# Kernel optimization log

Measured on AMD Instinct MI355X. Metric: run time of the kernel, lower is better.

## Reference

```python
import jax, jax.numpy as jnp
import numpy as np
from jax import lax

NUM_STEPS = 20
BATCH, DIM, HID = 4096, 512, 2048


def setup_inputs() -> dict:
    key = jax.random.key(0)
    k_z, k_w1, k_w2 = jax.random.split(key, 3)
    z0 = jax.random.normal(k_z, (BATCH, DIM), dtype=jnp.float32)
    # fan-in scaled weights so the ODE dynamics stay well-conditioned
    W1 = jax.random.normal(k_w1, (DIM + 1, HID), dtype=jnp.float32) * (1.0 / np.sqrt(DIM + 1))
    b1 = jnp.zeros((HID,), dtype=jnp.float32)
    W2 = jax.random.normal(k_w2, (HID, DIM), dtype=jnp.float32) * (0.1 / np.sqrt(HID))
    b2 = jnp.zeros((DIM,), dtype=jnp.float32)
    t0 = jnp.zeros((), dtype=jnp.float32)
    t1 = jnp.ones((), dtype=jnp.float32)
    return {"z0": z0, "W1": W1, "b1": b1, "W2": W2, "b2": b2, "t0": t0, "t1": t1}


def reference(z0, W1, b1, W2, b2, t0, t1):
    h = (t1 - t0) / NUM_STEPS

    def func(z, t):
        # time broadcast to [batch, 1], concatenated to the state (Neural-ODE MLP dynamics)
        tb = jnp.full((z.shape[0], 1), t, dtype=z.dtype)
        hidden = jnp.tanh(jnp.concatenate([z, tb], axis=-1) @ W1 + b1)
        return hidden @ W2 + b2

    def step(z, i):
        t = t0 + i * h
        k1 = func(z, t)
        k2 = func(z + 0.5 * h * k1, t + 0.5 * h)
        k3 = func(z + 0.5 * h * k2, t + 0.5 * h)
        k4 = func(z + h * k3, t + h)
        z_next = z + (h / 6.0) * (k1 + 2.0 * k2 + 2.0 * k3 + k4)
        return z_next, None

    z, _ = lax.scan(step, z0, jnp.arange(NUM_STEPS, dtype=z0.dtype))
    return z
```

## Files before the change

### kernel.cpp

```cpp
#include <hip/hip_runtime.h>
#include <hip/hip_bf16.h>

#define BATCH 4096
#define DIM   512
#define HID   2048
#define NSTEPS 20

typedef __attribute__((ext_vector_type(8))) short short8;
typedef __attribute__((ext_vector_type(4))) short short4v;
typedef __attribute__((ext_vector_type(4))) float floatx4;

#define GLL(dst, src) __builtin_amdgcn_global_load_lds( \
    (const __attribute__((address_space(1))) void*)(src), \
    (__attribute__((address_space(3))) void*)(dst), 16, 0, 0)

__device__ __forceinline__ short f2bf(float x) {
    union { float f; unsigned u; } v; v.f = x;
    unsigned r = v.u + 0x7fffu + ((v.u >> 16) & 1u);
    return (short)(r >> 16);
}

__device__ __forceinline__ float fast_tanh(float x) {
    float e = __builtin_amdgcn_exp2f(x * 2.8853900817779268f);
    float r = __builtin_amdgcn_rcpf(1.0f + e);
    return 1.0f - 2.0f * r;
}

__global__ void transpose_cvt(const float* __restrict__ src, short* __restrict__ dst,
                              int K, int N) {
    __shared__ float tile[32][33];
    int k0 = blockIdx.x * 32, n0 = blockIdx.y * 32;
    int tx = threadIdx.x, ty = threadIdx.y;
    #pragma unroll
    for (int r = ty; r < 32; r += 8)
        tile[r][tx] = src[(size_t)(k0 + r) * N + n0 + tx];
    __syncthreads();
    #pragma unroll
    for (int r = ty; r < 32; r += 8)
        dst[(size_t)(n0 + r) * K + k0 + tx] = f2bf(tile[tx][r]);
}

__global__ void extract_row(const float* __restrict__ W1, float* __restrict__ w1last) {
    int i = blockIdx.x * 256 + threadIdx.x;
    w1last[i] = W1[(size_t)DIM * HID + i];
}

__global__ void init_abuf(const float* __restrict__ z0, short* __restrict__ abuf) {
    size_t i = (size_t)(blockIdx.x * 256 + threadIdx.x) * 4;
    float4 zv = *(const float4*)(z0 + i);
    short4v o;
    o[0] = f2bf(zv.x); o[1] = f2bf(zv.y); o[2] = f2bf(zv.z); o[3] = f2bf(zv.w);
    *(short4v*)(abuf + i) = o;
}

__global__ __launch_bounds__(256, 2)
void gemm1_tanh(const short* __restrict__ A, const short* __restrict__ Bt,
                const float* __restrict__ b1, const float* __restrict__ w1last,
                const float* __restrict__ t0p, const float* __restrict__ t1p,
                float c_t, float step_i,
                short* __restrict__ hidden) {
    __shared__ short Alds[128 * 128];
    __shared__ short Blds[128 * 128];
    const int tid = threadIdx.x;
    const int lane = tid & 63;
    const int wave = tid >> 6;
    const int wm = wave >> 1, wn = wave & 1;
    const int bm0 = blockIdx.x * 128;
    const int bn0 = blockIdx.y * 128;

    const float t0 = t0p[0], t1 = t1p[0];
    const float h = (t1 - t0) / (float)NSTEPS;
    const float teval = t0 + (step_i + c_t) * h;

    floatx4 acc[4][4];
    #pragma unroll
    for (int i = 0; i < 4; i++)
        #pragma unroll
        for (int j = 0; j < 4; j++) acc[i][j] = (floatx4)0.f;

    const int fr = lane & 15;
    const int fkc = lane >> 4;
    const int rx = fr & 7;

    for (int kk = 0; kk < DIM; kk += 128) {
        #pragma unroll
        for (int p = 0; p < 8; p++) {
            int c = tid + p * 256;
            int row = c >> 4;
            int ci = c & 15;
            int g = ((ci & 7) ^ (row & 7)) | (ci & 8);
            GLL(&Alds[c * 8], A  + (size_t)(bm0 + row) * DIM + kk + g * 8);
            GLL(&Blds[c * 8], Bt + (size_t)(bn0 + row) * DIM + kk + g * 8);
        }
        __syncthreads();
        #pragma unroll
        for (int s = 0; s < 4; s++) {
            const int lc = s * 4 + fkc;
            const int slot = ((((lc & 7) ^ rx) | (lc & 8))) * 8;
            short8 af[4], bfr[4];
            #pragma unroll
            for (int mt = 0; mt < 4; mt++)
                af[mt] = *(const short8*)&Alds[(wm * 64 + mt * 16 + fr) * 128 + slot];
            #pragma unroll
            for (int nt = 0; nt < 4; nt++)
                bfr[nt] = *(const short8*)&Blds[(wn * 64 + nt * 16 + fr) * 128 + slot];
            #pragma unroll
            for (int mt = 0; mt < 4; mt++)
                #pragma unroll
                for (int nt = 0; nt < 4; nt++)
                    acc[mt][nt] = __builtin_amdgcn_mfma_f32_16x16x32_bf16(bfr[nt], af[mt], acc[mt][nt], 0, 0, 0);
        }
        __syncthreads();
    }
    #pragma unroll
    for (int mt = 0; mt < 4; mt++) {
        int m = bm0 + wm * 64 + mt * 16 + fr;
        short* hrow = hidden + (size_t)m * HID;
        #pragma unroll
        for (int nt = 0; nt < 4; nt++) {
            int n0 = bn0 + wn * 64 + nt * 16 + fkc * 4;
            float4 bb = *(const float4*)&b1[n0];
            float4 wl = *(const float4*)&w1last[n0];
            short4v o;
            o[0] = f2bf(fast_tanh(acc[mt][nt][0] + bb.x + teval * wl.x));
            o[1] = f2bf(fast_tanh(acc[mt][nt][1] + bb.y + teval * wl.y));
            o[2] = f2bf(fast_tanh(acc[mt][nt][2] + bb.z + teval * wl.z));
            o[3] = f2bf(fast_tanh(acc[mt][nt][3] + bb.w + teval * wl.w));
            *(short4v*)&hrow[n0] = o;
        }
    }
}

__global__ __launch_bounds__(512, 2)
void gemm2_fused(const short* __restrict__ hidden,
                 const short* __restrict__ Bt,
                 const float* __restrict__ b2,
                 float* __restrict__ z,
                 float* __restrict__ kacc, short* __restrict__ abuf,
                 const float* __restrict__ t0p, const float* __restrict__ t1p,
                 int mode, float wk, float alpha_c) {
    __shared__ short lds[8 * 8192];
    const int tid = threadIdx.x;
    const int lane = tid & 63;
    const int wave = tid >> 6;
    const int bm0 = blockIdx.x * 64;
    const int bn0 = blockIdx.y * 64;
    const int kbase = wave * 256;

    short* slabA = &lds[wave * 8192];
    short* slabB = slabA + 4096;

    const int fr = lane & 15;
    const int fkc = lane >> 4;
    const int rx = fr & 7;
    const int l3 = lane >> 3;
    const int gch = (lane & 7) ^ l3;

    floatx4 acc[4][4];
    #pragma unroll
    for (int i = 0; i < 4; i++)
        #pragma unroll
        for (int j = 0; j < 4; j++) acc[i][j] = (floatx4)0.f;

    #pragma unroll
    for (int it = 0; it < 4; ++it) {
        const int k0 = kbase + it * 64;
        __builtin_amdgcn_s_waitcnt(0xC07F);
        #pragma unroll
        for (int j = 0; j < 8; j++) {
            int row = j * 8 + l3;
            GLL(&slabA[j * 512 + lane * 8], hidden + (size_t)(bm0 + row) * HID + k0 + gch * 8);
            GLL(&slabB[j * 512 + lane * 8], Bt     + (size_t)(bn0 + row) * HID + k0 + gch * 8);
        }
        __builtin_amdgcn_sched_barrier(0);
        __builtin_amdgcn_s_waitcnt(0x0F70);
        __builtin_amdgcn_sched_barrier(0);
        #pragma unroll
        for (int s = 0; s < 2; s++) {
            const int slot = ((s * 4 + fkc) ^ rx) * 8;
            short8 af[4], bfr[4];
            #pragma unroll
            for (int mt = 0; mt < 4; mt++)
                af[mt] = *(const short8*)&slabA[(mt * 16 + fr) * 64 + slot];
            #pragma unroll
            for (int nt = 0; nt < 4; nt++)
                bfr[nt] = *(const short8*)&slabB[(nt * 16 + fr) * 64 + slot];
            #pragma unroll
            for (int mt = 0; mt < 4; mt++)
                #pragma unroll
                for (int nt = 0; nt < 4; nt++)
                    acc[mt][nt] = __builtin_amdgcn_mfma_f32_16x16x32_bf16(af[mt], bfr[nt], acc[mt][nt], 0, 0, 0);
        }
        __builtin_amdgcn_sched_barrier(0);
    }

    float* fslab = (float*)slabA;
    #pragma unroll
    for (int mt = 0; mt < 4; mt++)
        #pragma unroll
        for (int nt = 0; nt < 4; nt++)
            #pragma unroll
            for (int r = 0; r < 4; r++) {
                int row = mt * 16 + fkc * 4 + r;
                int col = nt * 16 + fr;
                fslab[row * 64 + col] = acc[mt][nt][r];
            }
    __syncthreads();

    const int rrow = tid >> 3;
    const int c8 = (tid & 7) * 8;
    float4 v0 = make_float4(0.f, 0.f, 0.f, 0.f);
    float4 v1 = make_float4(0.f, 0.f, 0.f, 0.f);
    #pragma unroll
    for (int w = 0; w < 8; w++) {
        const float* fs = (const float*)&lds[w * 8192];
        float4 p0 = *(const float4*)&fs[rrow * 64 + c8];
        float4 p1 = *(const float4*)&fs[rrow * 64 + c8 + 4];
        v0.x += p0.x; v0.y += p0.y; v0.z += p0.z; v0.w += p0.w;
        v1.x += p1.x; v1.y += p1.y; v1.z += p1.z; v1.w += p1.w;
    }

    const float h = (t1p[0] - t0p[0]) / (float)NSTEPS;
    const float ah = alpha_c * h;
    const float h6 = h / 6.0f;
    const size_t base = (size_t)(bm0 + rrow) * DIM + bn0 + c8;
    float4 bb0 = *(const float4*)&b2[bn0 + c8];
    float4 bb1 = *(const float4*)&b2[bn0 + c8 + 4];
    float kv[8] = { v0.x + bb0.x, v0.y + bb0.y, v0.z + bb0.z, v0.w + bb0.w,
                    v1.x + bb1.x, v1.y + bb1.y, v1.z + bb1.z, v1.w + bb1.w };
    float4 zv0 = *(const float4*)&z[base];
    float4 zv1 = *(const float4*)&z[base + 4];
    float zl[8] = { zv0.x, zv0.y, zv0.z, zv0.w, zv1.x, zv1.y, zv1.z, zv1.w };
    float zn[8];
    if (mode == 0) {
        *(float4*)&kacc[base]     = make_float4(kv[0], kv[1], kv[2], kv[3]);
        *(float4*)&kacc[base + 4] = make_float4(kv[4], kv[5], kv[6], kv[7]);
        #pragma unroll
        for (int i = 0; i < 8; i++) zn[i] = zl[i] + ah * kv[i];
    } else if (mode == 1) {
        float4 ka0 = *(const float4*)&kacc[base];
        float4 ka1 = *(const float4*)&kacc[base + 4];
        *(float4*)&kacc[base]     = make_float4(ka0.x + wk * kv[0], ka0.y + wk * kv[1],
                                                ka0.z + wk * kv[2], ka0.w + wk * kv[3]);
        *(float4*)&kacc[base + 4] = make_float4(ka1.x + wk * kv[4], ka1.y + wk * kv[5],
                                                ka1.z + wk * kv[6], ka1.w + wk * kv[7]);
        #pragma unroll
        for (int i = 0; i < 8; i++) zn[i] = zl[i] + ah * kv[i];
    } else {
        float4 ka0 = *(const float4*)&kacc[base];
        float4 ka1 = *(const float4*)&kacc[base + 4];
        float kaf[8] = { ka0.x, ka0.y, ka0.z, ka0.w, ka1.x, ka1.y, ka1.z, ka1.w };
        #pragma unroll
        for (int i = 0; i < 8; i++) zn[i] = zl[i] + h6 * (kaf[i] + kv[i]);
        *(float4*)&z[base]     = make_float4(zn[0], zn[1], zn[2], zn[3]);
        *(float4*)&z[base + 4] = make_float4(zn[4], zn[5], zn[6], zn[7]);
    }
    short4v o0, o1;
    o0[0] = f2bf(zn[0]); o0[1] = f2bf(zn[1]); o0[2] = f2bf(zn[2]); o0[3] = f2bf(zn[3]);
    o1[0] = f2bf(zn[4]); o1[1] = f2bf(zn[5]); o1[2] = f2bf(zn[6]); o1[3] = f2bf(zn[7]);
    *(short4v*)&abuf[base]     = o0;
    *(short4v*)&abuf[base + 4] = o1;
}

extern "C" void kernel_launch(void* const* d_in, const int* in_sizes, int n_in,
                              void* d_out, int out_size, void* d_ws, size_t ws_size,
                              hipStream_t stream) {
    const float* z0  = (const float*)d_in[0];
    const float* W1  = (const float*)d_in[1];
    const float* b1  = (const float*)d_in[2];
    const float* W2  = (const float*)d_in[3];
    const float* b2  = (const float*)d_in[4];
    const float* t0p = (const float*)d_in[5];
    const float* t1p = (const float*)d_in[6];
    float* z = (float*)d_out;

    char* ws = (char*)d_ws;
    short* W1t    = (short*)(ws);
    short* W2t    = (short*)(ws + (2u << 20));
    float* w1last = (float*)(ws + (4u << 20));
    short* abuf   = (short*)(ws + (4u << 20) + (1u << 16));
    short* hidden = (short*)(ws + (8u << 20) + (1u << 16));
    float* kacc   = (float*)(ws + (24u << 20) + (1u << 16));

    hipMemcpyAsync(z, z0, (size_t)BATCH * DIM * sizeof(float),
                   hipMemcpyDeviceToDevice, stream);
    transpose_cvt<<<dim3(DIM / 32, HID / 32), dim3(32, 8), 0, stream>>>(W1, W1t, DIM, HID);
    transpose_cvt<<<dim3(HID / 32, DIM / 32), dim3(32, 8), 0, stream>>>(W2, W2t, HID, DIM);
    extract_row<<<HID / 256, 256, 0, stream>>>(W1, w1last);
    init_abuf<<<BATCH * DIM / 4 / 256, 256, 0, stream>>>(z0, abuf);

    const dim3 g1(BATCH / 128, HID / 128), g2(BATCH / 64, DIM / 64);
    const dim3 b1d(256), b2d(512);
    for (int i = 0; i < NSTEPS; i++) {
        float fi = (float)i;
        gemm1_tanh<<<g1, b1d, 0, stream>>>(abuf, W1t, b1, w1last, t0p, t1p, 0.0f, fi, hidden);
        gemm2_fused<<<g2, b2d, 0, stream>>>(hidden, W2t, b2, z, kacc, abuf, t0p, t1p, 0, 1.0f, 0.5f);
        gemm1_tanh<<<g1, b1d, 0, stream>>>(abuf, W1t, b1, w1last, t0p, t1p, 0.5f, fi, hidden);
        gemm2_fused<<<g2, b2d, 0, stream>>>(hidden, W2t, b2, z, kacc, abuf, t0p, t1p, 1, 2.0f, 0.5f);
        gemm1_tanh<<<g1, b1d, 0, stream>>>(abuf, W1t, b1, w1last, t0p, t1p, 0.5f, fi, hidden);
        gemm2_fused<<<g2, b2d, 0, stream>>>(hidden, W2t, b2, z, kacc, abuf, t0p, t1p, 1, 2.0f, 1.0f);
        gemm1_tanh<<<g1, b1d, 0, stream>>>(abuf, W1t, b1, w1last, t0p, t1p, 1.0f, fi, hidden);
        gemm2_fused<<<g2, b2d, 0, stream>>>(hidden, W2t, b2, z, kacc, abuf, t0p, t1p, 2, 1.0f, 0.0f);
    }
}
```

Before: 2.958 ms.

## Double-buffer GEMM K-loops, swizzle block order, halve gemm2 split-K waves

In gemm1, the 128-wide K tiles become double-buffered 64-wide tiles so the next global-to-LDS load overlaps the current MFMAs and one barrier per iteration is dropped. In gemm2, the kernel moves from 8 to 4 waves per block, each wave taking a longer K range with 32-wide double-buffered slabs. Both kernels remap block indices with an XCD-aware swizzle to improve L2 locality. The gemm2 epilogue reduction uses an XOR-swizzled LDS layout with 16 outputs per thread. The risks are less parallelism inside each gemm2 block and hand-coded waitcnt values that have to stay correct.

```diff
diff --git a/kernel.cpp b/kernel.cpp
--- a/kernel.cpp
+++ b/kernel.cpp
@@ -59,14 +59,17 @@
                 const float* __restrict__ t0p, const float* __restrict__ t1p,
                 float c_t, float step_i,
                 short* __restrict__ hidden) {
-    __shared__ short Alds[128 * 128];
-    __shared__ short Blds[128 * 128];
+    __shared__ short Alds[2][128 * 64];
+    __shared__ short Blds[2][128 * 64];
     const int tid = threadIdx.x;
     const int lane = tid & 63;
     const int wave = tid >> 6;
     const int wm = wave >> 1, wn = wave & 1;
-    const int bm0 = blockIdx.x * 128;
-    const int bn0 = blockIdx.y * 128;
+
+    const int f = blockIdx.x + gridDim.x * blockIdx.y;
+    const int swz = (f & 7) * 64 + (f >> 3);
+    const int bm0 = (swz >> 4) * 128;
+    const int bn0 = (swz & 15) * 128;
 
     const float t0 = t0p[0], t1 = t1p[0];
     const float h = (t1 - t0) / (float)NSTEPS;
@@ -82,35 +85,40 @@
     const int fkc = lane >> 4;
     const int rx = fr & 7;
 
-    for (int kk = 0; kk < DIM; kk += 128) {
-        #pragma unroll
-        for (int p = 0; p < 8; p++) {
-            int c = tid + p * 256;
-            int row = c >> 4;
-            int ci = c & 15;
-            int g = ((ci & 7) ^ (row & 7)) | (ci & 8);
-            GLL(&Alds[c * 8], A  + (size_t)(bm0 + row) * DIM + kk + g * 8);
-            GLL(&Blds[c * 8], Bt + (size_t)(bn0 + row) * DIM + kk + g * 8);
-        }
-        __syncthreads();
-        #pragma unroll
-        for (int s = 0; s < 4; s++) {
+    #define STAGE1(buf, kk) do { \
+        _Pragma("unroll") \
+        for (int p = 0; p < 4; p++) { \
+            const int l = tid + p * 256; \
+            const int row = l >> 3; \
+            const int g = (l & 7) ^ (row & 7); \
+            GLL(&Alds[(buf)][l * 8], A  + (size_t)(bm0 + row) * DIM + (kk) + g * 8); \
+            GLL(&Blds[(buf)][l * 8], Bt + (size_t)(bn0 + row) * DIM + (kk) + g * 8); \
+        } } while (0)
+
+    STAGE1(0, 0);
+    __syncthreads();
+    #pragma unroll
+    for (int it = 0; it < 8; ++it) {
+        const int cur = it & 1;
+        if (it < 7) STAGE1(cur ^ 1, (it + 1) * 64);
+        #pragma unroll
+        for (int s = 0; s < 2; s++) {
             const int lc = s * 4 + fkc;
-            const int slot = ((((lc & 7) ^ rx) | (lc & 8))) * 8;
+            const int slot = (lc ^ rx) * 8;
             short8 af[4], bfr[4];
             #pragma unroll
             for (int mt = 0; mt < 4; mt++)
-                af[mt] = *(const short8*)&Alds[(wm * 64 + mt * 16 + fr) * 128 + slot];
+                af[mt] = *(const short8*)&Alds[cur][(wm * 64 + mt * 16 + fr) * 64 + slot];
             #pragma unroll
             for (int nt = 0; nt < 4; nt++)
-                bfr[nt] = *(const short8*)&Blds[(wn * 64 + nt * 16 + fr) * 128 + slot];
+                bfr[nt] = *(const short8*)&Blds[cur][(wn * 64 + nt * 16 + fr) * 64 + slot];
             #pragma unroll
             for (int mt = 0; mt < 4; mt++)
                 #pragma unroll
                 for (int nt = 0; nt < 4; nt++)
                     acc[mt][nt] = __builtin_amdgcn_mfma_f32_16x16x32_bf16(bfr[nt], af[mt], acc[mt][nt], 0, 0, 0);
         }
-        __syncthreads();
+        if (it < 7) __syncthreads();
     }
     #pragma unroll
     for (int mt = 0; mt < 4; mt++) {
@@ -131,7 +139,7 @@
     }
 }
 
-__global__ __launch_bounds__(512, 2)
+__global__ __launch_bounds__(256, 2)
 void gemm2_fused(const short* __restrict__ hidden,
                  const short* __restrict__ Bt,
                  const float* __restrict__ b2,
@@ -139,22 +147,21 @@
                  float* __restrict__ kacc, short* __restrict__ abuf,
                  const float* __restrict__ t0p, const float* __restrict__ t1p,
                  int mode, float wk, float alpha_c) {
-    __shared__ short lds[8 * 8192];
+    __shared__ short lds[4 * 8192];
     const int tid = threadIdx.x;
     const int lane = tid & 63;
     const int wave = tid >> 6;
-    const int bm0 = blockIdx.x * 64;
-    const int bn0 = blockIdx.y * 64;
-    const int kbase = wave * 256;
-
-    short* slabA = &lds[wave * 8192];
-    short* slabB = slabA + 4096;
+
+    const int f = blockIdx.x + gridDim.x * blockIdx.y;
+    const int swz = (f & 7) * 64 + (f >> 3);
+    const int bm0 = (swz >> 3) * 64;
+    const int bn0 = (swz & 7) * 64;
+    const int kbase = wave * 512;
+
+    short* slab = &lds[wave * 8192];
 
     const int fr = lane & 15;
     const int fkc = lane >> 4;
-    const int rx = fr & 7;
-    const int l3 = lane >> 3;
-    const int gch = (lane & 7) ^ l3;
 
     floatx4 acc[4][4];
     #pragma unroll
@@ -162,39 +169,50 @@
         #pragma unroll
         for (int j = 0; j < 4; j++) acc[i][j] = (floatx4)0.f;
 
-    #pragma unroll
-    for (int it = 0; it < 4; ++it) {
-        const int k0 = kbase + it * 64;
-        __builtin_amdgcn_s_waitcnt(0xC07F);
-        #pragma unroll
-        for (int j = 0; j < 8; j++) {
-            int row = j * 8 + l3;
-            GLL(&slabA[j * 512 + lane * 8], hidden + (size_t)(bm0 + row) * HID + k0 + gch * 8);
-            GLL(&slabB[j * 512 + lane * 8], Bt     + (size_t)(bn0 + row) * HID + k0 + gch * 8);
-        }
-        __builtin_amdgcn_sched_barrier(0);
-        __builtin_amdgcn_s_waitcnt(0x0F70);
-        __builtin_amdgcn_sched_barrier(0);
-        #pragma unroll
-        for (int s = 0; s < 2; s++) {
-            const int slot = ((s * 4 + fkc) ^ rx) * 8;
-            short8 af[4], bfr[4];
-            #pragma unroll
-            for (int mt = 0; mt < 4; mt++)
-                af[mt] = *(const short8*)&slabA[(mt * 16 + fr) * 64 + slot];
+    #define STAGE2(b, k0) do { \
+        _Pragma("unroll") \
+        for (int j = 0; j < 4; j++) { \
+            const int row = j * 16 + (lane >> 2); \
+            const int g = (lane & 3) ^ ((lane >> 3) & 3); \
+            GLL(slab + (b) * 4096 +        (j * 64 + lane) * 8, \
+                hidden + (size_t)(bm0 + row) * HID + (k0) + g * 8); \
+            GLL(slab + (b) * 4096 + 2048 + (j * 64 + lane) * 8, \
+                Bt     + (size_t)(bn0 + row) * HID + (k0) + g * 8); \
+        } } while (0)
+
+    STAGE2(0, kbase);
+    #pragma unroll
+    for (int it = 0; it < 16; ++it) {
+        const int cur = it & 1;
+        if (it < 15) {
+            STAGE2(cur ^ 1, kbase + (it + 1) * 32);
+            __builtin_amdgcn_sched_barrier(0);
+            __builtin_amdgcn_s_waitcnt(0x0F78);
+            __builtin_amdgcn_sched_barrier(0);
+        } else {
+            __builtin_amdgcn_sched_barrier(0);
+            __builtin_amdgcn_s_waitcnt(0x0F70);
+            __builtin_amdgcn_sched_barrier(0);
+        }
+        const short* sa = slab + cur * 4096;
+        const short* sb = sa + 2048;
+        const int phys = (fkc ^ ((fr >> 1) & 3)) * 8;
+        short8 af[4], bfr[4];
+        #pragma unroll
+        for (int mt = 0; mt < 4; mt++)
+            af[mt] = *(const short8*)&sa[(mt * 16 + fr) * 32 + phys];
+        #pragma unroll
+        for (int nt = 0; nt < 4; nt++)
+            bfr[nt] = *(const short8*)&sb[(nt * 16 + fr) * 32 + phys];
+        #pragma unroll
+        for (int mt = 0; mt < 4; mt++)
             #pragma unroll
             for (int nt = 0; nt < 4; nt++)
-                bfr[nt] = *(const short8*)&slabB[(nt * 16 + fr) * 64 + slot];
-            #pragma unroll
-            for (int mt = 0; mt < 4; mt++)
-                #pragma unroll
-                for (int nt = 0; nt < 4; nt++)
-                    acc[mt][nt] = __builtin_amdgcn_mfma_f32_16x16x32_bf16(af[mt], bfr[nt], acc[mt][nt], 0, 0, 0);
-        }
-        __builtin_amdgcn_sched_barrier(0);
-    }
-
-    float* fslab = (float*)slabA;
+                acc[mt][nt] = __builtin_amdgcn_mfma_f32_16x16x32_bf16(af[mt], bfr[nt], acc[mt][nt], 0, 0, 0);
+    }
+
+    __builtin_amdgcn_s_waitcnt(0xC07F);
+    float* fslab = (float*)slab;
     #pragma unroll
     for (int mt = 0; mt < 4; mt++)
         #pragma unroll
@@ -203,63 +221,78 @@
             for (int r = 0; r < 4; r++) {
                 int row = mt * 16 + fkc * 4 + r;
                 int col = nt * 16 + fr;
-                fslab[row * 64 + col] = acc[mt][nt][r];
+                int pc4 = (col >> 2) ^ (row & 15);
+                fslab[row * 64 + pc4 * 4 + (col & 3)] = acc[mt][nt][r];
             }
     __syncthreads();
 
-    const int rrow = tid >> 3;
-    const int c8 = (tid & 7) * 8;
-    float4 v0 = make_float4(0.f, 0.f, 0.f, 0.f);
-    float4 v1 = make_float4(0.f, 0.f, 0.f, 0.f);
-    #pragma unroll
-    for (int w = 0; w < 8; w++) {
+    const int rrow = tid >> 2;
+    const int cc = tid & 3;
+    float4 v[4];
+    #pragma unroll
+    for (int q = 0; q < 4; q++) v[q] = make_float4(0.f, 0.f, 0.f, 0.f);
+    #pragma unroll
+    for (int w = 0; w < 4; w++) {
         const float* fs = (const float*)&lds[w * 8192];
-        float4 p0 = *(const float4*)&fs[rrow * 64 + c8];
-        float4 p1 = *(const float4*)&fs[rrow * 64 + c8 + 4];
-        v0.x += p0.x; v0.y += p0.y; v0.z += p0.z; v0.w += p0.w;
-        v1.x += p1.x; v1.y += p1.y; v1.z += p1.z; v1.w += p1.w;
-    }
-
-    const float h = (t1p[0] - t0p[0]) / (float)NSTEPS;
-    const float ah = alpha_c * h;
-    const float h6 = h / 6.0f;
-    const size_t base = (size_t)(bm0 + rrow) * DIM + bn0 + c8;
-    float4 bb0 = *(const float4*)&b2[bn0 + c8];
-    float4 bb1 = *(const float4*)&b2[bn0 + c8 + 4];
-    float kv[8] = { v0.x + bb0.x, v0.y + bb0.y, v0.z + bb0.z, v0.w + bb0.w,
-                    v1.x + bb1.x, v1.y + bb1.y, v1.z + bb1.z, v1.w + bb1.w };
-    float4 zv0 = *(const float4*)&z[base];
-    float4 zv1 = *(const float4*)&z[base + 4];
-    float zl[8] = { zv0.x, zv0.y, zv0.z, zv0.w, zv1.x, zv1.y, zv1.z, zv1.w };
-    float zn[8];
+        #pragma unroll
+        for (int q = 0; q < 4; q++) {
+            int pc4 = (cc * 4 + q) ^ (rrow & 15);
+            float4 p = *(const float4*)&fs[rrow * 64 + pc4 * 4];
+            v[q].x += p.x; v[q].y += p.y; v[q].z += p.z; v[q].w += p.w;
+        }
+    }
+
+    const float hh = (t1p[0] - t0p[0]) / (float)NSTEPS;
+    const float ah = alpha_c * hh;
+    const float h6 = hh / 6.0f;
+    const size_t base = (size_t)(bm0 + rrow) * DIM + bn0 + cc * 16;
+
+    float kv[16], zl[16], zn[16];
+    #pragma unroll
+    for (int q = 0; q < 4; q++) {
+        float4 bb = *(const float4*)&b2[bn0 + cc * 16 + q * 4];
+        kv[q * 4 + 0] = v[q].x + bb.x;
+        kv[q * 4 + 1] = v[q].y + bb.y;
+        kv[q * 4 + 2] = v[q].z + bb.z;
+        kv[q * 4 + 3] = v[q].w + bb.w;
+        float4 zq = *(const float4*)&z[base + q * 4];
+        zl[q * 4 + 0] = zq.x; zl[q * 4 + 1] = zq.y;
+        zl[q * 4 + 2] = zq.z; zl[q * 4 + 3] = zq.w;
+    }
     if (mode == 0) {
-        *(float4*)&kacc[base]     = make_float4(kv[0], kv[1], kv[2], kv[3]);
-        *(float4*)&kacc[base + 4] = make_float4(kv[4], kv[5], kv[6], kv[7]);
-        #pragma unroll
-        for (int i = 0; i < 8; i++) zn[i] = zl[i] + ah * kv[i];
+        #pragma unroll
+        for (int q = 0; q < 4; q++)
+            *(float4*)&kacc[base + q * 4] =
+                make_float4(kv[q*4], kv[q*4+1], kv[q*4+2], kv[q*4+3]);
+        #pragma unroll
+        for (int i = 0; i < 16; i++) zn[i] = zl[i] + ah * kv[i];
     } else if (mode == 1) {
-        float4 ka0 = *(const float4*)&kacc[base];
-        float4 ka1 = *(const float4*)&kacc[base + 4];
-        *(float4*)&kacc[base]     = make_float4(ka0.x + wk * kv[0], ka0.y + wk * kv[1],
-                                                ka0.z + wk * kv[2], ka0.w + wk * kv[3]);
-        *(float4*)&kacc[base + 4] = make_float4(ka1.x + wk * kv[4], ka1.y + wk * kv[5],
-                                                ka1.z + wk * kv[6], ka1.w + wk * kv[7]);
-        #pragma unroll
-        for (int i = 0; i < 8; i++) zn[i] = zl[i] + ah * kv[i];
+        #pragma unroll
+        for (int q = 0; q < 4; q++) {
+            float4 ka = *(const float4*)&kacc[base + q * 4];
+            *(float4*)&kacc[base + q * 4] =
+                make_float4(ka.x + wk * kv[q*4],   ka.y + wk * kv[q*4+1],
+                            ka.z + wk * kv[q*4+2], ka.w + wk * kv[q*4+3]);
+        }
+        #pragma unroll
+        for (int i = 0; i < 16; i++) zn[i] = zl[i] + ah * kv[i];
     } else {
-        float4 ka0 = *(const float4*)&kacc[base];
-        float4 ka1 = *(const float4*)&kacc[base + 4];
-        float kaf[8] = { ka0.x, ka0.y, ka0.z, ka0.w, ka1.x, ka1.y, ka1.z, ka1.w };
-        #pragma unroll
-        for (int i = 0; i < 8; i++) zn[i] = zl[i] + h6 * (kaf[i] + kv[i]);
-        *(float4*)&z[base]     = make_float4(zn[0], zn[1], zn[2], zn[3]);
-        *(float4*)&z[base + 4] = make_float4(zn[4], zn[5], zn[6], zn[7]);
-    }
-    short4v o0, o1;
-    o0[0] = f2bf(zn[0]); o0[1] = f2bf(zn[1]); o0[2] = f2bf(zn[2]); o0[3] = f2bf(zn[3]);
-    o1[0] = f2bf(zn[4]); o1[1] = f2bf(zn[5]); o1[2] = f2bf(zn[6]); o1[3] = f2bf(zn[7]);
-    *(short4v*)&abuf[base]     = o0;
-    *(short4v*)&abuf[base + 4] = o1;
+        #pragma unroll
+        for (int q = 0; q < 4; q++) {
+            float4 ka = *(const float4*)&kacc[base + q * 4];
+            zn[q*4+0] = zl[q*4+0] + h6 * (ka.x + kv[q*4+0]);
+            zn[q*4+1] = zl[q*4+1] + h6 * (ka.y + kv[q*4+1]);
+            zn[q*4+2] = zl[q*4+2] + h6 * (ka.z + kv[q*4+2]);
+            zn[q*4+3] = zl[q*4+3] + h6 * (ka.w + kv[q*4+3]);
+            *(float4*)&z[base + q * 4] =
+                make_float4(zn[q*4], zn[q*4+1], zn[q*4+2], zn[q*4+3]);
+        }
+    }
+    short8 o0, o1;
+    #pragma unroll
+    for (int i = 0; i < 8; i++) { o0[i] = f2bf(zn[i]); o1[i] = f2bf(zn[8 + i]); }
+    *(short8*)&abuf[base] = o0;
+    *(short8*)&abuf[base + 8] = o1;
 }
 
 extern "C" void kernel_launch(void* const* d_in, const int* in_sizes, int n_in,
@@ -290,7 +323,7 @@
     init_abuf<<<BATCH * DIM / 4 / 256, 256, 0, stream>>>(z0, abuf);
 
     const dim3 g1(BATCH / 128, HID / 128), g2(BATCH / 64, DIM / 64);
-    const dim3 b1d(256), b2d(512);
+    const dim3 b1d(256), b2d(256);
     for (int i = 0; i < NSTEPS; i++) {
         float fi = (float)i;
         gemm1_tanh<<<g1, b1d, 0, stream>>>(abuf, W1t, b1, w1last, t0p, t1p, 0.0f, fi, hidden);
```

Result: slower. 3.462 ms (+17.1%).

## Enlarge gemm2 M tile to 128 rows with two accumulator sets sharing B fragments

Applied to the files above, without the earlier changes.

The split-K second GEMM now computes a 128x64 output tile per block instead of 64x64. It keeps two accumulator arrays that reuse the same B fragments, and uses 32-wide K chunks with a new LDS swizzle. The cross-wave reduction and RK4 epilogue run twice, once per 64-row half, reusing the LDS scratch. This halves the grid and W2 tile reloads per output row, but doubles accumulator registers under launch_bounds(512,2), which may cause spills or lower occupancy, and adds an extra reduction pass and barriers.

```diff
diff --git a/kernel.cpp b/kernel.cpp
--- a/kernel.cpp
+++ b/kernel.cpp
@@ -139,127 +139,149 @@
                  float* __restrict__ kacc, short* __restrict__ abuf,
                  const float* __restrict__ t0p, const float* __restrict__ t1p,
                  int mode, float wk, float alpha_c) {
-    __shared__ short lds[8 * 8192];
+    __shared__ short lds[65536];
     const int tid = threadIdx.x;
     const int lane = tid & 63;
     const int wave = tid >> 6;
-    const int bm0 = blockIdx.x * 64;
+    const int bm0 = blockIdx.x * 128;
     const int bn0 = blockIdx.y * 64;
     const int kbase = wave * 256;
 
-    short* slabA = &lds[wave * 8192];
-    short* slabB = slabA + 4096;
+    short* slabA0 = &lds[wave * 6144];
+    short* slabA1 = slabA0 + 2048;
+    short* slabB  = slabA0 + 4096;
 
     const int fr = lane & 15;
     const int fkc = lane >> 4;
-    const int rx = fr & 7;
-    const int l3 = lane >> 3;
-    const int gch = (lane & 7) ^ l3;
-
-    floatx4 acc[4][4];
+    const int l2b = (lane >> 3) & 3;
+    const int gch = (lane & 3) ^ l2b;
+    const int srow = lane >> 2;
+    const int phys = (fkc ^ ((fr >> 1) & 3)) * 8;
+
+    floatx4 acc0[4][4], acc1[4][4];
     #pragma unroll
     for (int i = 0; i < 4; i++)
         #pragma unroll
-        for (int j = 0; j < 4; j++) acc[i][j] = (floatx4)0.f;
-
-    #pragma unroll
-    for (int it = 0; it < 4; ++it) {
-        const int k0 = kbase + it * 64;
+        for (int j = 0; j < 4; j++) { acc0[i][j] = (floatx4)0.f; acc1[i][j] = (floatx4)0.f; }
+
+    #pragma unroll
+    for (int it = 0; it < 8; ++it) {
+        const int k0 = kbase + it * 32;
         __builtin_amdgcn_s_waitcnt(0xC07F);
-        #pragma unroll
-        for (int j = 0; j < 8; j++) {
-            int row = j * 8 + l3;
-            GLL(&slabA[j * 512 + lane * 8], hidden + (size_t)(bm0 + row) * HID + k0 + gch * 8);
-            GLL(&slabB[j * 512 + lane * 8], Bt     + (size_t)(bn0 + row) * HID + k0 + gch * 8);
+        __builtin_amdgcn_sched_barrier(0);
+        #pragma unroll
+        for (int j = 0; j < 4; j++) {
+            const int row = j * 16 + srow;
+            GLL(&slabA0[j * 512 + lane * 8], hidden + (size_t)(bm0 + row) * HID + k0 + gch * 8);
+            GLL(&slabA1[j * 512 + lane * 8], hidden + (size_t)(bm0 + 64 + row) * HID + k0 + gch * 8);
+            GLL(&slabB [j * 512 + lane * 8], Bt     + (size_t)(bn0 + row) * HID + k0 + gch * 8);
         }
         __builtin_amdgcn_sched_barrier(0);
         __builtin_amdgcn_s_waitcnt(0x0F70);
         __builtin_amdgcn_sched_barrier(0);
-        #pragma unroll
-        for (int s = 0; s < 2; s++) {
-            const int slot = ((s * 4 + fkc) ^ rx) * 8;
-            short8 af[4], bfr[4];
-            #pragma unroll
-            for (int mt = 0; mt < 4; mt++)
-                af[mt] = *(const short8*)&slabA[(mt * 16 + fr) * 64 + slot];
-            #pragma unroll
-            for (int nt = 0; nt < 4; nt++)
-                bfr[nt] = *(const short8*)&slabB[(nt * 16 + fr) * 64 + slot];
+        short8 bfrg[4];
+        #pragma unroll
+        for (int nt = 0; nt < 4; nt++)
+            bfrg[nt] = *(const short8*)&slabB[(nt * 16 + fr) * 32 + phys];
+        {
+            short8 af[4];
+            #pragma unroll
+            for (int mt = 0; mt < 4; mt++)
+                af[mt] = *(const short8*)&slabA0[(mt * 16 + fr) * 32 + phys];
             #pragma unroll
             for (int mt = 0; mt < 4; mt++)
                 #pragma unroll
                 for (int nt = 0; nt < 4; nt++)
-                    acc[mt][nt] = __builtin_amdgcn_mfma_f32_16x16x32_bf16(af[mt], bfr[nt], acc[mt][nt], 0, 0, 0);
+                    acc0[mt][nt] = __builtin_amdgcn_mfma_f32_16x16x32_bf16(af[mt], bfrg[nt], acc0[mt][nt], 0, 0, 0);
+        }
+        {
+            short8 af[4];
+            #pragma unroll
+            for (int mt = 0; mt < 4; mt++)
+                af[mt] = *(const short8*)&slabA1[(mt * 16 + fr) * 32 + phys];
+            #pragma unroll
+            for (int mt = 0; mt < 4; mt++)
+                #pragma unroll
+                for (int nt = 0; nt < 4; nt++)
+                    acc1[mt][nt] = __builtin_amdgcn_mfma_f32_16x16x32_bf16(af[mt], bfrg[nt], acc1[mt][nt], 0, 0, 0);
         }
         __builtin_amdgcn_sched_barrier(0);
     }
 
-    float* fslab = (float*)slabA;
-    #pragma unroll
-    for (int mt = 0; mt < 4; mt++)
-        #pragma unroll
-        for (int nt = 0; nt < 4; nt++)
-            #pragma unroll
-            for (int r = 0; r < 4; r++) {
-                int row = mt * 16 + fkc * 4 + r;
-                int col = nt * 16 + fr;
-                fslab[row * 64 + col] = acc[mt][nt][r];
-            }
+    __builtin_amdgcn_s_waitcnt(0xC07F);
     __syncthreads();
 
+    const float hh = (t1p[0] - t0p[0]) / (float)NSTEPS;
+    const float ah = alpha_c * hh;
+    const float h6 = hh / 6.0f;
     const int rrow = tid >> 3;
     const int c8 = (tid & 7) * 8;
-    float4 v0 = make_float4(0.f, 0.f, 0.f, 0.f);
-    float4 v1 = make_float4(0.f, 0.f, 0.f, 0.f);
-    #pragma unroll
-    for (int w = 0; w < 8; w++) {
-        const float* fs = (const float*)&lds[w * 8192];
-        float4 p0 = *(const float4*)&fs[rrow * 64 + c8];
-        float4 p1 = *(const float4*)&fs[rrow * 64 + c8 + 4];
-        v0.x += p0.x; v0.y += p0.y; v0.z += p0.z; v0.w += p0.w;
-        v1.x += p1.x; v1.y += p1.y; v1.z += p1.z; v1.w += p1.w;
-    }
-
-    const float h = (t1p[0] - t0p[0]) / (float)NSTEPS;
-    const float ah = alpha_c * h;
-    const float h6 = h / 6.0f;
-    const size_t base = (size_t)(bm0 + rrow) * DIM + bn0 + c8;
     float4 bb0 = *(const float4*)&b2[bn0 + c8];
     float4 bb1 = *(const float4*)&b2[bn0 + c8 + 4];
-    float kv[8] = { v0.x + bb0.x, v0.y + bb0.y, v0.z + bb0.z, v0.w + bb0.w,
-                    v1.x + bb1.x, v1.y + bb1.y, v1.z + bb1.z, v1.w + bb1.w };
-    float4 zv0 = *(const float4*)&z[base];
-    float4 zv1 = *(const float4*)&z[base + 4];
-    float zl[8] = { zv0.x, zv0.y, zv0.z, zv0.w, zv1.x, zv1.y, zv1.z, zv1.w };
-    float zn[8];
-    if (mode == 0) {
-        *(float4*)&kacc[base]     = make_float4(kv[0], kv[1], kv[2], kv[3]);
-        *(float4*)&kacc[base + 4] = make_float4(kv[4], kv[5], kv[6], kv[7]);
-        #pragma unroll
-        for (int i = 0; i < 8; i++) zn[i] = zl[i] + ah * kv[i];
-    } else if (mode == 1) {
-        float4 ka0 = *(const float4*)&kacc[base];
-        float4 ka1 = *(const float4*)&kacc[base + 4];
-        *(float4*)&kacc[base]     = make_float4(ka0.x + wk * kv[0], ka0.y + wk * kv[1],
-                                                ka0.z + wk * kv[2], ka0.w + wk * kv[3]);
-        *(float4*)&kacc[base + 4] = make_float4(ka1.x + wk * kv[4], ka1.y + wk * kv[5],
-                                                ka1.z + wk * kv[6], ka1.w + wk * kv[7]);
-        #pragma unroll
-        for (int i = 0; i < 8; i++) zn[i] = zl[i] + ah * kv[i];
-    } else {
-        float4 ka0 = *(const float4*)&kacc[base];
-        float4 ka1 = *(const float4*)&kacc[base + 4];
-        float kaf[8] = { ka0.x, ka0.y, ka0.z, ka0.w, ka1.x, ka1.y, ka1.z, ka1.w };
-        #pragma unroll
-        for (int i = 0; i < 8; i++) zn[i] = zl[i] + h6 * (kaf[i] + kv[i]);
-        *(float4*)&z[base]     = make_float4(zn[0], zn[1], zn[2], zn[3]);
-        *(float4*)&z[base + 4] = make_float4(zn[4], zn[5], zn[6], zn[7]);
-    }
-    short4v o0, o1;
-    o0[0] = f2bf(zn[0]); o0[1] = f2bf(zn[1]); o0[2] = f2bf(zn[2]); o0[3] = f2bf(zn[3]);
-    o1[0] = f2bf(zn[4]); o1[1] = f2bf(zn[5]); o1[2] = f2bf(zn[6]); o1[3] = f2bf(zn[7]);
-    *(short4v*)&abuf[base]     = o0;
-    *(short4v*)&abuf[base + 4] = o1;
+
+    #pragma unroll
+    for (int mh = 0; mh < 2; mh++) {
+        float* fslab = (float*)&lds[wave * 8192];
+        #pragma unroll
+        for (int mt = 0; mt < 4; mt++)
+            #pragma unroll
+            for (int nt = 0; nt < 4; nt++)
+                #pragma unroll
+                for (int r = 0; r < 4; r++) {
+                    int row = mt * 16 + fkc * 4 + r;
+                    int col = nt * 16 + fr;
+                    fslab[row * 64 + col] = (mh == 0) ? acc0[mt][nt][r] : acc1[mt][nt][r];
+                }
+        __syncthreads();
+
+        float4 v0 = make_float4(0.f, 0.f, 0.f, 0.f);
+        float4 v1 = make_float4(0.f, 0.f, 0.f, 0.f);
+        #pragma unroll
+        for (int w = 0; w < 8; w++) {
+            const float* fs = (const float*)&lds[w * 8192];
+            float4 p0 = *(const float4*)&fs[rrow * 64 + c8];
+            float4 p1 = *(const float4*)&fs[rrow * 64 + c8 + 4];
+            v0.x += p0.x; v0.y += p0.y; v0.z += p0.z; v0.w += p0.w;
+            v1.x += p1.x; v1.y += p1.y; v1.z += p1.z; v1.w += p1.w;
+        }
+
+        const size_t base = (size_t)(bm0 + mh * 64 + rrow) * DIM + bn0 + c8;
+        float kv[8] = { v0.x + bb0.x, v0.y + bb0.y, v0.z + bb0.z, v0.w + bb0.w,
+                        v1.x + bb1.x, v1.y + bb1.y, v1.z + bb1.z, v1.w + bb1.w };
+        float4 zv0 = *(const float4*)&z[base];
+        float4 zv1 = *(const float4*)&z[base + 4];
+        float zl[8] = { zv0.x, zv0.y, zv0.z, zv0.w, zv1.x, zv1.y, zv1.z, zv1.w };
+        float zn[8];
+        if (mode == 0) {
+            *(float4*)&kacc[base]     = make_float4(kv[0], kv[1], kv[2], kv[3]);
+            *(float4*)&kacc[base + 4] = make_float4(kv[4], kv[5], kv[6], kv[7]);
+            #pragma unroll
+            for (int i = 0; i < 8; i++) zn[i] = zl[i] + ah * kv[i];
+        } else if (mode == 1) {
+            float4 ka0 = *(const float4*)&kacc[base];
+            float4 ka1 = *(const float4*)&kacc[base + 4];
+            *(float4*)&kacc[base]     = make_float4(ka0.x + wk * kv[0], ka0.y + wk * kv[1],
+                                                    ka0.z + wk * kv[2], ka0.w + wk * kv[3]);
+            *(float4*)&kacc[base + 4] = make_float4(ka1.x + wk * kv[4], ka1.y + wk * kv[5],
+                                                    ka1.z + wk * kv[6], ka1.w + wk * kv[7]);
+            #pragma unroll
+            for (int i = 0; i < 8; i++) zn[i] = zl[i] + ah * kv[i];
+        } else {
+            float4 ka0 = *(const float4*)&kacc[base];
+            float4 ka1 = *(const float4*)&kacc[base + 4];
+            float kaf[8] = { ka0.x, ka0.y, ka0.z, ka0.w, ka1.x, ka1.y, ka1.z, ka1.w };
+            #pragma unroll
+            for (int i = 0; i < 8; i++) zn[i] = zl[i] + h6 * (kaf[i] + kv[i]);
+            *(float4*)&z[base]     = make_float4(zn[0], zn[1], zn[2], zn[3]);
+            *(float4*)&z[base + 4] = make_float4(zn[4], zn[5], zn[6], zn[7]);
+        }
+        short4v o0, o1;
+        o0[0] = f2bf(zn[0]); o0[1] = f2bf(zn[1]); o0[2] = f2bf(zn[2]); o0[3] = f2bf(zn[3]);
+        o1[0] = f2bf(zn[4]); o1[1] = f2bf(zn[5]); o1[2] = f2bf(zn[6]); o1[3] = f2bf(zn[7]);
+        *(short4v*)&abuf[base]     = o0;
+        *(short4v*)&abuf[base + 4] = o1;
+        if (mh == 0) __syncthreads();
+    }
 }
 
 extern "C" void kernel_launch(void* const* d_in, const int* in_sizes, int n_in,
@@ -289,7 +311,7 @@
     extract_row<<<HID / 256, 256, 0, stream>>>(W1, w1last);
     init_abuf<<<BATCH * DIM / 4 / 256, 256, 0, stream>>>(z0, abuf);
 
-    const dim3 g1(BATCH / 128, HID / 128), g2(BATCH / 64, DIM / 64);
+    const dim3 g1(BATCH / 128, HID / 128), g2(BATCH / 128, DIM / 64);
     const dim3 b1d(256), b2d(512);
     for (int i = 0; i < NSTEPS; i++) {
         float fi = (float)i;
```

New measurement: 3.158 ms. 1.07x slower.

## Double-buffer gemm1 LDS with 256x128 tiles and 512-thread blocks

Applied to the files above, without the earlier changes.

Reworks the first GEMM (z·W1 + tanh) to use 256x128 block tiles with 8 waves. K is staged in 64-wide chunks into two LDS buffers, so global-to-LDS loads for chunk t+2 overlap with MFMA work on the current chunk. Explicit waitcnt, sched_barrier and setprio around the MFMA bursts control the interleaving. This trades occupancy (one 512-thread block per CU) and half the number of blocks for less load stall per block and more reuse of the B tile.

```diff
diff --git a/kernel.cpp b/kernel.cpp
--- a/kernel.cpp
+++ b/kernel.cpp
@@ -53,19 +53,20 @@
     *(short4v*)(abuf + i) = o;
 }
 
-__global__ __launch_bounds__(256, 2)
+__global__ __launch_bounds__(512, 1)
 void gemm1_tanh(const short* __restrict__ A, const short* __restrict__ Bt,
                 const float* __restrict__ b1, const float* __restrict__ w1last,
                 const float* __restrict__ t0p, const float* __restrict__ t1p,
                 float c_t, float step_i,
                 short* __restrict__ hidden) {
-    __shared__ short Alds[128 * 128];
-    __shared__ short Blds[128 * 128];
+    __shared__ short Alds[2][256 * 64];
+    __shared__ short Blds[2][128 * 64];
     const int tid = threadIdx.x;
     const int lane = tid & 63;
     const int wave = tid >> 6;
-    const int wm = wave >> 1, wn = wave & 1;
-    const int bm0 = blockIdx.x * 128;
+    const int wm = wave >> 1;
+    const int wn = wave & 1;
+    const int bm0 = blockIdx.x * 256;
     const int bn0 = blockIdx.y * 128;
 
     const float t0 = t0p[0], t1 = t1p[0];
@@ -82,36 +83,67 @@
     const int fkc = lane >> 4;
     const int rx = fr & 7;
 
-    for (int kk = 0; kk < DIM; kk += 128) {
-        #pragma unroll
-        for (int p = 0; p < 8; p++) {
-            int c = tid + p * 256;
-            int row = c >> 4;
-            int ci = c & 15;
-            int g = ((ci & 7) ^ (row & 7)) | (ci & 8);
-            GLL(&Alds[c * 8], A  + (size_t)(bm0 + row) * DIM + kk + g * 8);
-            GLL(&Blds[c * 8], Bt + (size_t)(bn0 + row) * DIM + kk + g * 8);
-        }
-        __syncthreads();
-        #pragma unroll
-        for (int s = 0; s < 4; s++) {
+    #define STAGE1(buf, kk) do { \
+        _Pragma("unroll") \
+        for (int p = 0; p < 4; p++) { \
+            const int c = tid + p * 512; \
+            const int row = c >> 3; \
+            const int g = (c & 7) ^ (row & 7); \
+            GLL(&Alds[(buf)][c * 8], A + (size_t)(bm0 + row) * DIM + (kk) + g * 8); \
+        } \
+        _Pragma("unroll") \
+        for (int p = 0; p < 2; p++) { \
+            const int c = tid + p * 512; \
+            const int row = c >> 3; \
+            const int g = (c & 7) ^ (row & 7); \
+            GLL(&Blds[(buf)][c * 8], Bt + (size_t)(bn0 + row) * DIM + (kk) + g * 8); \
+        } } while (0)
+
+    STAGE1(0, 0);
+    STAGE1(1, 64);
+    __builtin_amdgcn_sched_barrier(0);
+    __builtin_amdgcn_s_waitcnt(0x0F76);
+    __builtin_amdgcn_sched_barrier(0);
+    __builtin_amdgcn_s_barrier();
+
+    #pragma unroll
+    for (int t = 0; t < 8; ++t) {
+        const int cur = t & 1;
+        #pragma unroll
+        for (int s = 0; s < 2; s++) {
             const int lc = s * 4 + fkc;
-            const int slot = ((((lc & 7) ^ rx) | (lc & 8))) * 8;
+            const int slot = (lc ^ rx) * 8;
             short8 af[4], bfr[4];
             #pragma unroll
             for (int mt = 0; mt < 4; mt++)
-                af[mt] = *(const short8*)&Alds[(wm * 64 + mt * 16 + fr) * 128 + slot];
+                af[mt] = *(const short8*)&Alds[cur][(wm * 64 + mt * 16 + fr) * 64 + slot];
             #pragma unroll
             for (int nt = 0; nt < 4; nt++)
-                bfr[nt] = *(const short8*)&Blds[(wn * 64 + nt * 16 + fr) * 128 + slot];
+                bfr[nt] = *(const short8*)&Blds[cur][(wn * 64 + nt * 16 + fr) * 64 + slot];
+            __builtin_amdgcn_s_setprio(1);
             #pragma unroll
             for (int mt = 0; mt < 4; mt++)
                 #pragma unroll
                 for (int nt = 0; nt < 4; nt++)
                     acc[mt][nt] = __builtin_amdgcn_mfma_f32_16x16x32_bf16(bfr[nt], af[mt], acc[mt][nt], 0, 0, 0);
-        }
-        __syncthreads();
-    }
+            __builtin_amdgcn_s_setprio(0);
+        }
+        __builtin_amdgcn_sched_barrier(0);
+        __builtin_amdgcn_s_barrier();
+        if (t < 6) {
+            STAGE1(cur, (t + 2) * 64);
+            __builtin_amdgcn_sched_barrier(0);
+            __builtin_amdgcn_s_waitcnt(0x0F76);
+            __builtin_amdgcn_sched_barrier(0);
+            __builtin_amdgcn_s_barrier();
+        } else if (t == 6) {
+            __builtin_amdgcn_sched_barrier(0);
+            __builtin_amdgcn_s_waitcnt(0x0F70);
+            __builtin_amdgcn_sched_barrier(0);
+            __builtin_amdgcn_s_barrier();
+        }
+    }
+
     #pragma unroll
     for (int mt = 0; mt < 4; mt++) {
         int m = bm0 + wm * 64 + mt * 16 + fr;
@@ -289,8 +321,8 @@
     extract_row<<<HID / 256, 256, 0, stream>>>(W1, w1last);
     init_abuf<<<BATCH * DIM / 4 / 256, 256, 0, stream>>>(z0, abuf);
 
-    const dim3 g1(BATCH / 128, HID / 128), g2(BATCH / 64, DIM / 64);
-    const dim3 b1d(256), b2d(512);
+    const dim3 g1(BATCH / 256, HID / 128), g2(BATCH / 64, DIM / 64);
+    const dim3 b1d(512), b2d(512);
     for (int i = 0; i < NSTEPS; i++) {
         float fi = (float)i;
         gemm1_tanh<<<g1, b1d, 0, stream>>>(abuf, W1t, b1, w1last, t0p, t1p, 0.0f, fi, hidden);
```

Result: slower. 3.191 ms (+7.9%).
